# Performance work log

Measured on AMD Instinct MI355X. Metric: run time of the kernel, lower is better.

Reference implementation:

```python
import jax, jax.numpy as jnp
import numpy as np

B, H, S, D = 1, 16, 4096, 64

def setup_inputs() -> dict:
    key = jax.random.key(0)
    kq, kk, kv = jax.random.split(key, 3)
    q = jax.random.normal(kq, (B, H, S, D), dtype=jnp.float32)
    k = jax.random.normal(kk, (B, H, S, D), dtype=jnp.float32)
    v = jax.random.normal(kv, (B, H, S, D), dtype=jnp.float32)
    # causal mask, broadcastable over batch and heads: True = attend
    mask = jnp.tril(jnp.ones((S, S), dtype=bool))[None, None, :, :]
    return {"q": q, "k": k, "v": v, "mask": mask}


def reference(q, k, v, mask):
    # Chunked attention in the original is mathematically identical to full
    # attention: each query-chunk softmaxes over ALL keys. Vectorized form:
    dim_head = q.shape[-1]
    scale = 1.0 / jnp.sqrt(jnp.asarray(dim_head, dtype=q.dtype))
    scores = jnp.einsum("bhqd,bhkd->bhqk", q, k) * scale  # [B,H,S,S]
    scores = jnp.where(mask, scores, -jnp.inf)
    attn = jax.nn.softmax(scores, axis=-1)
    attn = jnp.nan_to_num(attn, nan=0.0)  # rows with all keys masked -> 0
    return jnp.einsum("bhqk,bhkd->bhqd", attn, v)
```

## Files before the change

kernel.cpp:

```cpp
#include <hip/hip_runtime.h>
#include <hip/hip_bf16.h>
#include <math.h>


typedef __bf16 bf16;
typedef __bf16 bf16x8 __attribute__((ext_vector_type(8)));
typedef float f32x16 __attribute__((ext_vector_type(16)));

#define NH 16
#define SEQ 4096
#define DH 64
#define QB 128
#define WQ 32
#define KB 128
#define LOG2E 1.44269504088896340736f

static __device__ __forceinline__ void mfma32(f32x16& c, bf16x8 a, bf16x8 b) {
  asm("v_mfma_f32_32x32x16_bf16 %0, %1, %2, %0" : "+v"(c) : "v"(a), "v"(b));
}
static __device__ __forceinline__ float exp2a(float x) {
  float r; asm("v_exp_f32 %0, %1" : "=v"(r) : "v"(x)); return r;
}
static __device__ __forceinline__ unsigned pk(float lo, float hi) {
  unsigned r; asm("v_cvt_pk_bf16_f32 %0, %1, %2" : "=v"(r) : "v"(lo), "v"(hi)); return r;
}
static __device__ __forceinline__ void swap32(unsigned& a, unsigned& b) {
  asm("v_permlane32_swap_b32 %0, %1" : "+v"(a), "+v"(b));
}

union AFrag { unsigned u[4]; bf16x8 v; };

static __device__ __forceinline__ bf16x8 cvt8(float4 a, float4 b) {
  bf16x8 f;
  f[0]=(bf16)a.x; f[1]=(bf16)a.y; f[2]=(bf16)a.z; f[3]=(bf16)a.w;
  f[4]=(bf16)b.x; f[5]=(bf16)b.y; f[6]=(bf16)b.z; f[7]=(bf16)b.w;
  return f;
}

__global__ __launch_bounds__(256, 2)
void fa_fwd(const float* __restrict__ Q, const float* __restrict__ K,
            const float* __restrict__ V, float* __restrict__ O) {
  __shared__ bf16 Ksh[2][KB * DH];
  __shared__ bf16 Vts[2][DH * KB];

  const int bid  = blockIdx.x;
  const int head = bid & (NH - 1);
  const int qblk = (SEQ / QB - 1) - (bid >> 4);
  const int qb   = qblk * QB;

  const int tid = threadIdx.x;
  const int w   = tid >> 6;
  const int l   = tid & 63;
  const int lc  = l & 31;
  const int hi  = l >> 5;
  const int qw  = qb + w * WQ;
  const int qv  = qw + lc;

  const float* Qh = Q + (size_t)head * SEQ * DH;
  const float* Kh = K + (size_t)head * SEQ * DH;
  const float* Vh = V + (size_t)head * SEQ * DH;

  bf16x8 qf[4];
  {
    const float* qp = Qh + (size_t)qv * DH + hi * 8;
    const float sc = 0.125f * LOG2E;
#pragma unroll
    for (int ch = 0; ch < 4; ++ch) {
      float4 x = *(const float4*)(qp + ch * 16);
      float4 y = *(const float4*)(qp + ch * 16 + 4);
      bf16x8 f;
      f[0]=(bf16)(x.x*sc); f[1]=(bf16)(x.y*sc); f[2]=(bf16)(x.z*sc); f[3]=(bf16)(x.w*sc);
      f[4]=(bf16)(y.x*sc); f[5]=(bf16)(y.y*sc); f[6]=(bf16)(y.z*sc); f[7]=(bf16)(y.w*sc);
      qf[ch] = f;
    }
  }

  f32x16 o0 = {}, o1 = {};
  float m = -INFINITY, ls = 0.f;

  const int kr = tid >> 1, kc = (tid & 1) * 32;
  const int dg = tid & 7,  kp2 = tid >> 3;

  float4 kreg[8], vreg[8];
  const int nt = qblk + 1;

  {
    const float* p = Kh + (size_t)kr * DH + kc;
#pragma unroll
    for (int i = 0; i < 8; ++i) kreg[i] = ((const float4*)p)[i];
#pragma unroll
    for (int u = 0; u < 2; ++u) {
      const float* pv = Vh + (size_t)(2 * (kp2 + 32 * u)) * DH + dg * 8;
      vreg[u*4+0] = ((const float4*)pv)[0];
      vreg[u*4+1] = ((const float4*)pv)[1];
      vreg[u*4+2] = ((const float4*)(pv + DH))[0];
      vreg[u*4+3] = ((const float4*)(pv + DH))[1];
    }
  }

  for (int t = 0; t < nt; ++t) {
    const int kb = t * KB;
    const int b  = t & 1;

    {
      const int Sk = (((kr & 7) ^ ((kr >> 3) & 7)) << 4);
#pragma unroll
      for (int q = 0; q < 4; ++q)
        *(bf16x8*)((char*)Ksh[b] + kr * 128 + ((kc * 2 + q * 16) ^ Sk)) =
            cvt8(kreg[2*q], kreg[2*q+1]);
      const int xbase = (kp2 * 4) ^ (dg << 4);
#pragma unroll
      for (int u = 0; u < 2; ++u) {
        const int xb = xbase + u * 128;
#pragma unroll
        for (int i = 0; i < 8; ++i) {
          const float lo = vreg[u*4 + (i >> 2)    ][i & 3];
          const float hv = vreg[u*4 + (i >> 2) + 2][i & 3];
          *(unsigned*)((char*)Vts[b] + (dg * 8 + i) * 256 + (xb ^ (i << 4))) =
              pk(lo, hv);
        }
      }
    }
    __syncthreads();

    if (t + 1 < nt) {
      const int kn = kb + KB;
      const float* p = Kh + (size_t)(kn + kr) * DH + kc;
#pragma unroll
      for (int i = 0; i < 8; ++i) kreg[i] = ((const float4*)p)[i];
#pragma unroll
      for (int u = 0; u < 2; ++u) {
        const float* pv = Vh + (size_t)(kn + 2 * (kp2 + 32 * u)) * DH + dg * 8;
        vreg[u*4+0] = ((const float4*)pv)[0];
        vreg[u*4+1] = ((const float4*)pv)[1];
        vreg[u*4+2] = ((const float4*)(pv + DH))[0];
        vreg[u*4+3] = ((const float4*)(pv + DH))[1];
      }
    }

#pragma unroll
    for (int hb = 0; hb < 2; ++hb) {
      if (kb + hb * 64 > qw + 31) continue;

      f32x16 st0 = {}, st1 = {};
#pragma unroll
      for (int kt = 0; kt < 2; ++kt) {
        const int row = hb * 64 + kt * 32;
        const int Sr  = (((lc & 7) ^ ((kt * 4 + (lc >> 3)) & 7)) << 4);
        f32x16& st = kt ? st1 : st0;
#pragma unroll
        for (int ch = 0; ch < 4; ++ch) {
          const bf16x8 kf = *(const bf16x8*)((const char*)Ksh[b] +
              (row + lc) * 128 + ((ch * 32 + hi * 16) ^ Sr));
          mfma32(st, kf, qf[ch]);
        }
      }

      if (kb + hb * 64 + 63 > qw) {
#pragma unroll
        for (int r = 0; r < 16; ++r) {
          const int kg = kb + hb * 64 + ((r & 3) + 8 * (r >> 2) + 4 * hi);
          if (kg > qv)      st0[r] = -INFINITY;
          if (kg + 32 > qv) st1[r] = -INFINITY;
        }
      }

      float acc[8];
#pragma unroll
      for (int i = 0; i < 8; ++i)
        acc[i] = fmaxf(fmaxf(st0[i], st0[i + 8]), fmaxf(st1[i], st1[i + 8]));
      acc[0]=fmaxf(acc[0],acc[4]); acc[1]=fmaxf(acc[1],acc[5]);
      acc[2]=fmaxf(acc[2],acc[6]); acc[3]=fmaxf(acc[3],acc[7]);
      acc[0]=fmaxf(acc[0],acc[2]); acc[1]=fmaxf(acc[1],acc[3]);
      float mx = fmaxf(acc[0], acc[1]);
      mx = fmaxf(mx, __shfl_xor(mx, 32));

      if (__any(mx > m + 8.0f)) {
        const float mn = fmaxf(m, mx);
        const float al = exp2a(m - mn);
        m = mn;
        ls *= al;
#pragma unroll
        for (int r = 0; r < 16; ++r) {
          const float aq = __shfl(al, (r & 3) + 8 * (r >> 2) + 4 * hi);
          o0[r] *= aq; o1[r] *= aq;
        }
      }

      float rs = 0.f;
#pragma unroll
      for (int ks = 0; ks < 4; ++ks) {
        const f32x16& st = (ks < 2) ? st0 : st1;
        float p[8];
#pragma unroll
        for (int j = 0; j < 8; ++j) p[j] = exp2a(st[(ks & 1) * 8 + j] - m);
        rs += ((p[0]+p[1])+(p[2]+p[3])) + ((p[4]+p[5])+(p[6]+p[7]));
        unsigned u0 = pk(p[0],p[1]), u1 = pk(p[2],p[3]);
        unsigned u2 = pk(p[4],p[5]), u3 = pk(p[6],p[7]);
        swap32(u0, u2); swap32(u1, u3);
        AFrag af; af.u[0]=u0; af.u[1]=u1; af.u[2]=u2; af.u[3]=u3;
        const int koff = hb * 128 + ks * 32 + hi * 16;
        const int S0 = (((lc & 7) ^ ((lc >> 3) & 7)) << 4);
        const int S1 = (((lc & 7) ^ (((lc >> 3) + 4) & 7)) << 4);
        bf16x8 v0 = *(const bf16x8*)((const char*)Vts[b] +
            lc * 256 + (koff ^ S0));
        bf16x8 v1 = *(const bf16x8*)((const char*)Vts[b] +
            (lc + 32) * 256 + (koff ^ S1));
        mfma32(o0, af.v, v0);
        mfma32(o1, af.v, v1);
      }
      rs += __shfl_xor(rs, 32);
      ls += rs;
    }

    if (t + 1 < nt) __syncthreads();
  }

  const float inv = 1.0f / ls;
  float* Ob = O + (size_t)(head * SEQ + qw) * DH;
#pragma unroll
  for (int r = 0; r < 16; ++r) {
    const int row = (r & 3) + 8 * (r >> 2) + 4 * hi;
    const float iq = __shfl(inv, row);
    Ob[(size_t)row * DH + lc]      = o0[r] * iq;
    Ob[(size_t)row * DH + 32 + lc] = o1[r] * iq;
  }
}

extern "C" void kernel_launch(void* const* d_in, const int* in_sizes, int n_in,
                              void* d_out, int out_size, void* d_ws, size_t ws_size,
                              hipStream_t stream) {
  const float* q = (const float*)d_in[0];
  const float* k = (const float*)d_in[1];
  const float* v = (const float*)d_in[2];
  float* out = (float*)d_out;
  dim3 grid(NH * (SEQ / QB));
  dim3 block(256);
  fa_fwd<<<grid, block, 0, stream>>>(q, k, v, out);
}
```

Before: 221.9 us.

## Split long causal query blocks across KV halves with persistent atomic scheduler

Converts the grid to a persistent kernel that pulls work items from an atomic counter. Query blocks in the upper half of the sequence are split into two KV-range partials that write bf16 partial outputs plus max and sum to the workspace, and a separate combine kernel merges them. The goal is to fix load imbalance from the causal triangle, where the last query blocks do far more work than the first. In exchange it adds two extra kernel launches, workspace traffic, an atomic per item, and bf16 rounding of the partial outputs. The split path only runs if the workspace is large enough.

New measurement: 211.7 us. -4.6%, faster.

```diff
diff --git a/kernel.cpp b/kernel.cpp
--- a/kernel.cpp
+++ b/kernel.cpp
@@ -15,6 +15,13 @@
 #define KB 128
 #define LOG2E 1.44269504088896340736f
 
+#define NSLOT 512
+#define WS_O 256
+#define O_BYTES (NSLOT * 128 * 64 * 2)
+#define WS_M (WS_O + O_BYTES)
+#define WS_L (WS_M + NSLOT * 128 * 4)
+#define WS_NEED (WS_L + NSLOT * 128 * 4)
+
 static __device__ __forceinline__ void mfma32(f32x16& c, bf16x8 a, bf16x8 b) {
   asm("v_mfma_f32_32x32x16_bf16 %0, %1, %2, %0" : "+v"(c) : "v"(a), "v"(b));
 }
@@ -37,100 +44,84 @@
   return f;
 }
 
+__global__ void zero_ctr(unsigned* c) { if (threadIdx.x == 0) *c = 0; }
+
 __global__ __launch_bounds__(256, 2)
 void fa_fwd(const float* __restrict__ Q, const float* __restrict__ K,
-            const float* __restrict__ V, float* __restrict__ O) {
+            const float* __restrict__ V, float* __restrict__ O,
+            void* __restrict__ ws, const int nitems, const int split) {
   __shared__ bf16 Ksh[2][KB * DH];
   __shared__ bf16 Vts[2][DH * KB];
-
-  const int bid  = blockIdx.x;
-  const int head = bid & (NH - 1);
-  const int qblk = (SEQ / QB - 1) - (bid >> 4);
-  const int qb   = qblk * QB;
+  __shared__ int sh_item;
+
+  unsigned* ctr = (unsigned*)ws;
 
   const int tid = threadIdx.x;
   const int w   = tid >> 6;
   const int l   = tid & 63;
   const int lc  = l & 31;
   const int hi  = l >> 5;
-  const int qw  = qb + w * WQ;
-  const int qv  = qw + lc;
-
-  const float* Qh = Q + (size_t)head * SEQ * DH;
-  const float* Kh = K + (size_t)head * SEQ * DH;
-  const float* Vh = V + (size_t)head * SEQ * DH;
-
-  bf16x8 qf[4];
-  {
-    const float* qp = Qh + (size_t)qv * DH + hi * 8;
-    const float sc = 0.125f * LOG2E;
-#pragma unroll
-    for (int ch = 0; ch < 4; ++ch) {
-      float4 x = *(const float4*)(qp + ch * 16);
-      float4 y = *(const float4*)(qp + ch * 16 + 4);
-      bf16x8 f;
-      f[0]=(bf16)(x.x*sc); f[1]=(bf16)(x.y*sc); f[2]=(bf16)(x.z*sc); f[3]=(bf16)(x.w*sc);
-      f[4]=(bf16)(y.x*sc); f[5]=(bf16)(y.y*sc); f[6]=(bf16)(y.z*sc); f[7]=(bf16)(y.w*sc);
-      qf[ch] = f;
-    }
-  }
-
-  f32x16 o0 = {}, o1 = {};
-  float m = -INFINITY, ls = 0.f;
 
   const int kr = tid >> 1, kc = (tid & 1) * 32;
   const int dg = tid & 7,  kp2 = tid >> 3;
 
-  float4 kreg[8], vreg[8];
-  const int nt = qblk + 1;
-
-  {
-    const float* p = Kh + (size_t)kr * DH + kc;
-#pragma unroll
-    for (int i = 0; i < 8; ++i) kreg[i] = ((const float4*)p)[i];
-#pragma unroll
-    for (int u = 0; u < 2; ++u) {
-      const float* pv = Vh + (size_t)(2 * (kp2 + 32 * u)) * DH + dg * 8;
-      vreg[u*4+0] = ((const float4*)pv)[0];
-      vreg[u*4+1] = ((const float4*)pv)[1];
-      vreg[u*4+2] = ((const float4*)(pv + DH))[0];
-      vreg[u*4+3] = ((const float4*)(pv + DH))[1];
-    }
-  }
-
-  for (int t = 0; t < nt; ++t) {
-    const int kb = t * KB;
-    const int b  = t & 1;
-
+  for (;;) {
+    __syncthreads();
+    if (tid == 0) sh_item = (int)atomicAdd(ctr, 1u);
+    __syncthreads();
+    const int c = sh_item;
+    if (c >= nitems) break;
+
+    int head, qb, t0, t1, slot = -1;
+    if (!split) {
+      head = c & 15; const int qblk = 31 - (c >> 4);
+      qb = qblk * QB; t0 = 0; t1 = qblk + 1;
+    } else if (c < 256) {
+      head = c & 15; const int qblk = 16 + (c >> 4);
+      qb = qblk * QB; t0 = 0; t1 = 16;
+      slot = ((head << 4) + (qblk - 16)) * 2;
+    } else if (c < 512) {
+      const int i = c - 256; head = i & 15; const int qblk = 31 - (i >> 4);
+      qb = qblk * QB; t0 = 16; t1 = qblk + 1;
+      slot = ((head << 4) + (qblk - 16)) * 2 + 1;
+    } else {
+      const int i = c - 512; head = i & 15; const int qblk = 15 - (i >> 4);
+      qb = qblk * QB; t0 = 0; t1 = qblk + 1;
+    }
+
+    const int qw = qb + w * WQ;
+    const int qv = qw + lc;
+    const float* Qh = Q + (size_t)head * SEQ * DH;
+    const float* Kh = K + (size_t)head * SEQ * DH;
+    const float* Vh = V + (size_t)head * SEQ * DH;
+
+    bf16x8 qf[4];
     {
-      const int Sk = (((kr & 7) ^ ((kr >> 3) & 7)) << 4);
-#pragma unroll
-      for (int q = 0; q < 4; ++q)
-        *(bf16x8*)((char*)Ksh[b] + kr * 128 + ((kc * 2 + q * 16) ^ Sk)) =
-            cvt8(kreg[2*q], kreg[2*q+1]);
-      const int xbase = (kp2 * 4) ^ (dg << 4);
+      const float* qp = Qh + (size_t)qv * DH + hi * 8;
+      const float sc = 0.125f * LOG2E;
+#pragma unroll
+      for (int ch = 0; ch < 4; ++ch) {
+        float4 x = *(const float4*)(qp + ch * 16);
+        float4 y = *(const float4*)(qp + ch * 16 + 4);
+        bf16x8 f;
+        f[0]=(bf16)(x.x*sc); f[1]=(bf16)(x.y*sc); f[2]=(bf16)(x.z*sc); f[3]=(bf16)(x.w*sc);
+        f[4]=(bf16)(y.x*sc); f[5]=(bf16)(y.y*sc); f[6]=(bf16)(y.z*sc); f[7]=(bf16)(y.w*sc);
+        qf[ch] = f;
+      }
+    }
+
+    f32x16 o0 = {}, o1 = {};
+    float m = -INFINITY, ls = 0.f;
+
+    float4 kreg[8], vreg[8];
+    {
+      const int kb0 = t0 * KB;
+      const float* p = Kh + (size_t)(kb0 + kr) * DH + kc;
+#pragma unroll
+      for (int i = 0; i < 8; ++i) kreg[i] = ((const float4*)p)[i];
 #pragma unroll
       for (int u = 0; u < 2; ++u) {
-        const int xb = xbase + u * 128;
-#pragma unroll
-        for (int i = 0; i < 8; ++i) {
-          const float lo = vreg[u*4 + (i >> 2)    ][i & 3];
-          const float hv = vreg[u*4 + (i >> 2) + 2][i & 3];
-          *(unsigned*)((char*)Vts[b] + (dg * 8 + i) * 256 + (xb ^ (i << 4))) =
-              pk(lo, hv);
-        }
-      }
-    }
-    __syncthreads();
-
-    if (t + 1 < nt) {
-      const int kn = kb + KB;
-      const float* p = Kh + (size_t)(kn + kr) * DH + kc;
-#pragma unroll
-      for (int i = 0; i < 8; ++i) kreg[i] = ((const float4*)p)[i];
-#pragma unroll
-      for (int u = 0; u < 2; ++u) {
-        const float* pv = Vh + (size_t)(kn + 2 * (kp2 + 32 * u)) * DH + dg * 8;
+        const float* pv = Vh + (size_t)(kb0 + 2 * (kp2 + 32 * u)) * DH + dg * 8;
         vreg[u*4+0] = ((const float4*)pv)[0];
         vreg[u*4+1] = ((const float4*)pv)[1];
         vreg[u*4+2] = ((const float4*)(pv + DH))[0];
@@ -138,93 +129,174 @@
       }
     }
 
-#pragma unroll
-    for (int hb = 0; hb < 2; ++hb) {
-      if (kb + hb * 64 > qw + 31) continue;
-
-      f32x16 st0 = {}, st1 = {};
-#pragma unroll
-      for (int kt = 0; kt < 2; ++kt) {
-        const int row = hb * 64 + kt * 32;
-        const int Sr  = (((lc & 7) ^ ((kt * 4 + (lc >> 3)) & 7)) << 4);
-        f32x16& st = kt ? st1 : st0;
-#pragma unroll
-        for (int ch = 0; ch < 4; ++ch) {
-          const bf16x8 kf = *(const bf16x8*)((const char*)Ksh[b] +
-              (row + lc) * 128 + ((ch * 32 + hi * 16) ^ Sr));
-          mfma32(st, kf, qf[ch]);
-        }
-      }
-
-      if (kb + hb * 64 + 63 > qw) {
-#pragma unroll
-        for (int r = 0; r < 16; ++r) {
-          const int kg = kb + hb * 64 + ((r & 3) + 8 * (r >> 2) + 4 * hi);
-          if (kg > qv)      st0[r] = -INFINITY;
-          if (kg + 32 > qv) st1[r] = -INFINITY;
-        }
-      }
-
-      float acc[8];
-#pragma unroll
-      for (int i = 0; i < 8; ++i)
-        acc[i] = fmaxf(fmaxf(st0[i], st0[i + 8]), fmaxf(st1[i], st1[i + 8]));
-      acc[0]=fmaxf(acc[0],acc[4]); acc[1]=fmaxf(acc[1],acc[5]);
-      acc[2]=fmaxf(acc[2],acc[6]); acc[3]=fmaxf(acc[3],acc[7]);
-      acc[0]=fmaxf(acc[0],acc[2]); acc[1]=fmaxf(acc[1],acc[3]);
-      float mx = fmaxf(acc[0], acc[1]);
-      mx = fmaxf(mx, __shfl_xor(mx, 32));
-
-      if (__any(mx > m + 8.0f)) {
-        const float mn = fmaxf(m, mx);
-        const float al = exp2a(m - mn);
-        m = mn;
-        ls *= al;
-#pragma unroll
-        for (int r = 0; r < 16; ++r) {
-          const float aq = __shfl(al, (r & 3) + 8 * (r >> 2) + 4 * hi);
-          o0[r] *= aq; o1[r] *= aq;
-        }
-      }
-
-      float rs = 0.f;
-#pragma unroll
-      for (int ks = 0; ks < 4; ++ks) {
-        const f32x16& st = (ks < 2) ? st0 : st1;
-        float p[8];
-#pragma unroll
-        for (int j = 0; j < 8; ++j) p[j] = exp2a(st[(ks & 1) * 8 + j] - m);
-        rs += ((p[0]+p[1])+(p[2]+p[3])) + ((p[4]+p[5])+(p[6]+p[7]));
-        unsigned u0 = pk(p[0],p[1]), u1 = pk(p[2],p[3]);
-        unsigned u2 = pk(p[4],p[5]), u3 = pk(p[6],p[7]);
-        swap32(u0, u2); swap32(u1, u3);
-        AFrag af; af.u[0]=u0; af.u[1]=u1; af.u[2]=u2; af.u[3]=u3;
-        const int koff = hb * 128 + ks * 32 + hi * 16;
-        const int S0 = (((lc & 7) ^ ((lc >> 3) & 7)) << 4);
-        const int S1 = (((lc & 7) ^ (((lc >> 3) + 4) & 7)) << 4);
-        bf16x8 v0 = *(const bf16x8*)((const char*)Vts[b] +
-            lc * 256 + (koff ^ S0));
-        bf16x8 v1 = *(const bf16x8*)((const char*)Vts[b] +
-            (lc + 32) * 256 + (koff ^ S1));
-        mfma32(o0, af.v, v0);
-        mfma32(o1, af.v, v1);
-      }
-      rs += __shfl_xor(rs, 32);
-      ls += rs;
-    }
-
-    if (t + 1 < nt) __syncthreads();
+    for (int t = t0; t < t1; ++t) {
+      const int kb = t * KB;
+      const int b  = (t - t0) & 1;
+
+      {
+        const int Sk = (((kr & 7) ^ ((kr >> 3) & 7)) << 4);
+#pragma unroll
+        for (int q = 0; q < 4; ++q)
+          *(bf16x8*)((char*)Ksh[b] + kr * 128 + ((kc * 2 + q * 16) ^ Sk)) =
+              cvt8(kreg[2*q], kreg[2*q+1]);
+        const int xbase = (kp2 * 4) ^ (dg << 4);
+#pragma unroll
+        for (int u = 0; u < 2; ++u) {
+          const int xb = xbase + u * 128;
+#pragma unroll
+          for (int i = 0; i < 8; ++i) {
+            const float lo = vreg[u*4 + (i >> 2)    ][i & 3];
+            const float hv = vreg[u*4 + (i >> 2) + 2][i & 3];
+            *(unsigned*)((char*)Vts[b] + (dg * 8 + i) * 256 + (xb ^ (i << 4))) =
+                pk(lo, hv);
+          }
+        }
+      }
+      __syncthreads();
+
+      if (t + 1 < t1) {
+        const int kn = kb + KB;
+        const float* p = Kh + (size_t)(kn + kr) * DH + kc;
+#pragma unroll
+        for (int i = 0; i < 8; ++i) kreg[i] = ((const float4*)p)[i];
+#pragma unroll
+        for (int u = 0; u < 2; ++u) {
+          const float* pv = Vh + (size_t)(kn + 2 * (kp2 + 32 * u)) * DH + dg * 8;
+          vreg[u*4+0] = ((const float4*)pv)[0];
+          vreg[u*4+1] = ((const float4*)pv)[1];
+          vreg[u*4+2] = ((const float4*)(pv + DH))[0];
+          vreg[u*4+3] = ((const float4*)(pv + DH))[1];
+        }
+      }
+
+#pragma unroll
+      for (int hb = 0; hb < 2; ++hb) {
+        if (kb + hb * 64 > qw + 31) continue;
+
+        f32x16 st0 = {}, st1 = {};
+#pragma unroll
+        for (int kt = 0; kt < 2; ++kt) {
+          const int row = hb * 64 + kt * 32;
+          const int Sr  = (((lc & 7) ^ ((kt * 4 + (lc >> 3)) & 7)) << 4);
+          f32x16& st = kt ? st1 : st0;
+#pragma unroll
+          for (int ch = 0; ch < 4; ++ch) {
+            const bf16x8 kf = *(const bf16x8*)((const char*)Ksh[b] +
+                (row + lc) * 128 + ((ch * 32 + hi * 16) ^ Sr));
+            mfma32(st, kf, qf[ch]);
+          }
+        }
+
+        if (kb + hb * 64 + 63 > qw) {
+#pragma unroll
+          for (int r = 0; r < 16; ++r) {
+            const int kg = kb + hb * 64 + ((r & 3) + 8 * (r >> 2) + 4 * hi);
+            if (kg > qv)      st0[r] = -INFINITY;
+            if (kg + 32 > qv) st1[r] = -INFINITY;
+          }
+        }
+
+        float acc[8];
+#pragma unroll
+        for (int i = 0; i < 8; ++i)
+          acc[i] = fmaxf(fmaxf(st0[i], st0[i + 8]), fmaxf(st1[i], st1[i + 8]));
+        acc[0]=fmaxf(acc[0],acc[4]); acc[1]=fmaxf(acc[1],acc[5]);
+        acc[2]=fmaxf(acc[2],acc[6]); acc[3]=fmaxf(acc[3],acc[7]);
+        acc[0]=fmaxf(acc[0],acc[2]); acc[1]=fmaxf(acc[1],acc[3]);
+        float mx = fmaxf(acc[0], acc[1]);
+        mx = fmaxf(mx, __shfl_xor(mx, 32));
+
+        if (__any(mx > m + 8.0f)) {
+          const float mn = fmaxf(m, mx);
+          const float al = exp2a(m - mn);
+          m = mn;
+          ls *= al;
+#pragma unroll
+          for (int r = 0; r < 16; ++r) {
+            const float aq = __shfl(al, (r & 3) + 8 * (r >> 2) + 4 * hi);
+            o0[r] *= aq; o1[r] *= aq;
+          }
+        }
+
+        float rs = 0.f;
+#pragma unroll
+        for (int ks = 0; ks < 4; ++ks) {
+          const f32x16& st = (ks < 2) ? st0 : st1;
+          float p[8];
+#pragma unroll
+          for (int j = 0; j < 8; ++j) p[j] = exp2a(st[(ks & 1) * 8 + j] - m);
+          rs += ((p[0]+p[1])+(p[2]+p[3])) + ((p[4]+p[5])+(p[6]+p[7]));
+          unsigned u0 = pk(p[0],p[1]), u1 = pk(p[2],p[3]);
+          unsigned u2 = pk(p[4],p[5]), u3 = pk(p[6],p[7]);
+          swap32(u0, u2); swap32(u1, u3);
+          AFrag af; af.u[0]=u0; af.u[1]=u1; af.u[2]=u2; af.u[3]=u3;
+          const int koff = hb * 128 + ks * 32 + hi * 16;
+          const int S0 = (((lc & 7) ^ ((lc >> 3) & 7)) << 4);
+          const int S1 = (((lc & 7) ^ (((lc >> 3) + 4) & 7)) << 4);
+          bf16x8 v0 = *(const bf16x8*)((const char*)Vts[b] + lc * 256 + (koff ^ S0));
+          bf16x8 v1 = *(const bf16x8*)((const char*)Vts[b] + (lc + 32) * 256 + (koff ^ S1));
+          mfma32(o0, af.v, v0);
+          mfma32(o1, af.v, v1);
+        }
+        rs += __shfl_xor(rs, 32);
+        ls += rs;
+      }
+
+      if (t + 1 < t1) __syncthreads();
+    }
+
+    if (slot < 0) {
+      const float inv = 1.0f / ls;
+      float* Ob = O + (size_t)(head * SEQ + qw) * DH;
+#pragma unroll
+      for (int r = 0; r < 16; ++r) {
+        const int row = (r & 3) + 8 * (r >> 2) + 4 * hi;
+        const float iq = __shfl(inv, row);
+        Ob[(size_t)row * DH + lc]      = o0[r] * iq;
+        Ob[(size_t)row * DH + 32 + lc] = o1[r] * iq;
+      }
+    } else {
+      bf16* po = (bf16*)((char*)ws + WS_O) + (size_t)slot * (128 * 64);
+#pragma unroll
+      for (int r = 0; r < 16; ++r) {
+        const int row = w * WQ + (r & 3) + 8 * (r >> 2) + 4 * hi;
+        po[row * 64 + lc]      = (bf16)o0[r];
+        po[row * 64 + 32 + lc] = (bf16)o1[r];
+      }
+      if (hi == 0) {
+        ((float*)((char*)ws + WS_M))[slot * 128 + w * WQ + lc] = m;
+        ((float*)((char*)ws + WS_L))[slot * 128 + w * WQ + lc] = ls;
+      }
+    }
   }
-
-  const float inv = 1.0f / ls;
-  float* Ob = O + (size_t)(head * SEQ + qw) * DH;
-#pragma unroll
-  for (int r = 0; r < 16; ++r) {
-    const int row = (r & 3) + 8 * (r >> 2) + 4 * hi;
-    const float iq = __shfl(inv, row);
-    Ob[(size_t)row * DH + lc]      = o0[r] * iq;
-    Ob[(size_t)row * DH + 32 + lc] = o1[r] * iq;
-  }
+}
+
+__global__ __launch_bounds__(256)
+void fa_combine(float* __restrict__ O, const void* __restrict__ ws) {
+  const int idx   = blockIdx.x * 256 + threadIdx.x;
+  const int dpart = idx & 7;
+  const int row8  = idx >> 3;
+  const int r     = row8 & 127;
+  const int qb16  = (row8 >> 7) & 15;
+  const int h     = row8 >> 11;
+  const int s0    = ((h << 4) + qb16) * 2;
+
+  const float* pm = (const float*)((const char*)ws + WS_M);
+  const float* pl = (const float*)((const char*)ws + WS_L);
+  const float m0 = pm[s0 * 128 + r], m1 = pm[(s0 + 1) * 128 + r];
+  const float l0 = pl[s0 * 128 + r], l1 = pl[(s0 + 1) * 128 + r];
+  const float M  = fmaxf(m0, m1);
+  const float w0 = exp2f(m0 - M), w1 = exp2f(m1 - M);
+  const float inv = 1.0f / (l0 * w0 + l1 * w1);
+
+  const bf16* po = (const bf16*)((const char*)ws + WS_O);
+  const bf16x8 a = *(const bf16x8*)(po + (size_t)s0 * 8192 + r * 64 + dpart * 8);
+  const bf16x8 b = *(const bf16x8*)(po + (size_t)(s0 + 1) * 8192 + r * 64 + dpart * 8);
+
+  float* out = O + ((size_t)h * SEQ + (16 + qb16) * 128 + r) * DH + dpart * 8;
+#pragma unroll
+  for (int j = 0; j < 8; ++j)
+    out[j] = ((float)a[j] * w0 + (float)b[j] * w1) * inv;
 }
 
 extern "C" void kernel_launch(void* const* d_in, const int* in_sizes, int n_in,
@@ -234,7 +306,9 @@
   const float* k = (const float*)d_in[1];
   const float* v = (const float*)d_in[2];
   float* out = (float*)d_out;
-  dim3 grid(NH * (SEQ / QB));
-  dim3 block(256);
-  fa_fwd<<<grid, block, 0, stream>>>(q, k, v, out);
-}
+  const int split = (ws_size >= (size_t)WS_NEED) ? 1 : 0;
+
+  zero_ctr<<<1, 64, 0, stream>>>((unsigned*)d_ws);
+  fa_fwd<<<512, 256, 0, stream>>>(q, k, v, out, d_ws, split ? 768 : 512, split);
+  if (split) fa_combine<<<1024, 256, 0, stream>>>(out, d_ws);
+}
```
